# Kernel tuning notes

Measured on AMD Instinct MI355X. Metric: run time of the kernel, lower is better.

The kernel has to match this reference:

```python
import jax, jax.numpy as jnp
import numpy as np

B, L, CH = 8, 32768, 128   # segments, points per segment, channels
H, D = 4, 32               # num_head, ch_head (CH == H*D)
EPS = 1e-5                 # torch GroupNorm default eps


def group_norm1(x, w, b):
    # GroupNorm(num_groups=1, num_channels=CH) applied on [1, CH, L] per segment:
    # normalize over all channels AND points of each segment, then per-channel affine.
    mu = jnp.mean(x, axis=(1, 2), keepdims=True)            # [B,1,1]
    var = jnp.var(x, axis=(1, 2), keepdims=True)            # [B,1,1]
    return (x - mu) * jax.lax.rsqrt(var + EPS) * w + b      # [B,L,CH]


def setup_inputs() -> dict:
    key = jax.random.key(0)
    k0, k1, k2 = jax.random.split(key, 3)
    x = jax.random.normal(k0, (B, L, CH), dtype=jnp.float32)
    W_qkv = jax.random.normal(k1, (CH, 3 * H * D), dtype=jnp.float32) * 0.02
    W_out = jax.random.normal(k2, (H * D, CH), dtype=jnp.float32) * 0.02
    gn1_w = jnp.ones((CH,), jnp.float32)
    gn1_b = jnp.zeros((CH,), jnp.float32)
    gn2_w = jnp.ones((CH,), jnp.float32)
    gn2_b = jnp.zeros((CH,), jnp.float32)
    return {"x": x, "gn1_w": gn1_w, "gn1_b": gn1_b, "W_qkv": W_qkv,
            "W_out": W_out, "gn2_w": gn2_w, "gn2_b": gn2_b}


def reference(x, gn1_w, gn1_b, W_qkv, W_out, gn2_w, gn2_b):
    norm_x = group_norm1(x, gn1_w, gn1_b)                     # [B,L,CH]
    qkv = norm_x @ W_qkv                                      # [B,L,3*H*D]
    q, k, v = jnp.split(qkv, 3, axis=-1)
    q = q.reshape(B, L, H, D)
    k = k.reshape(B, L, H, D)
    v = v.reshape(B, L, H, D)
    # softmax over points within each segment (k / sqrt(segment_len))
    k_soft = jax.nn.softmax(k * (1.0 / np.float32(np.sqrt(L))), axis=1)
    # per-segment, per-head KV context: [B,H,D,D]
    context = jnp.einsum('blhk,blhv->bhkv', k_soft, v)
    # q scaled by ch_head**-0.5, softmax over feature dim
    q_soft = jax.nn.softmax(q * np.float32(D ** -0.5), axis=-1)
    out = jnp.einsum('blhk,bhkv->blhv', q_soft, context).reshape(B, L, H * D)
    out = out @ W_out                                          # [B,L,CH]
    out = group_norm1(out, gn2_w, gn2_b)
    return out + x  # residual
```

## Files before the change

### kernel.cpp

```cpp
#include <hip/hip_runtime.h>

#define NSEG 8
#define LSEG 32768
#define EPS_GN 1e-5f
#define KSCALE 0.005524271728019903f
#define QSCALE 0.17677669529663687f

typedef __attribute__((ext_vector_type(4))) float f32x4;
typedef __attribute__((ext_vector_type(8))) __bf16 bf16x8;
typedef __attribute__((ext_vector_type(4))) short s16x4;

static __device__ __forceinline__ unsigned short f2bf(float f) {
  unsigned int u = __float_as_uint(f);
  u += 0x7fffu + ((u >> 16) & 1u);
  return (unsigned short)(u >> 16);
}
static __device__ __forceinline__ float bf2f(unsigned short s) {
  return __uint_as_float(((unsigned int)s) << 16);
}
static __device__ __forceinline__ bf16x8 cvt8(float4 a, float4 b) {
  bf16x8 r;
  r[0] = (__bf16)a.x; r[1] = (__bf16)a.y; r[2] = (__bf16)a.z; r[3] = (__bf16)a.w;
  r[4] = (__bf16)b.x; r[5] = (__bf16)b.y; r[6] = (__bf16)b.z; r[7] = (__bf16)b.w;
  return r;
}
static __device__ __forceinline__ s16x4 pack4(float a, float b, float c, float d) {
  union { __bf16 h[4]; s16x4 s; } u;
  u.h[0] = (__bf16)a; u.h[1] = (__bf16)b; u.h[2] = (__bf16)c; u.h[3] = (__bf16)d;
  return u.s;
}
static __device__ __forceinline__ ushort4 packu4(f32x4 v) {
  union { __bf16 h[4]; ushort4 u; } u;
  u.h[0] = (__bf16)v[0]; u.h[1] = (__bf16)v[1]; u.h[2] = (__bf16)v[2]; u.h[3] = (__bf16)v[3];
  return u.u;
}

__global__ void k_wcvt(const float* __restrict__ W, const float* __restrict__ gn1w,
                       unsigned short* __restrict__ WT) {
  int idx = blockIdx.x * 256 + threadIdx.x;
  int n = idx >> 7, ch = idx & 127;
  WT[idx] = f2bf(gn1w[ch] * W[ch * 384 + n]);
}

__global__ __launch_bounds__(256) void k_stats1(const float* __restrict__ x, float* __restrict__ part) {
  int t = threadIdx.x;
  int b = blockIdx.x >> 6, p = blockIdx.x & 63;
  const float4* xp = (const float4*)x + (size_t)b * 1048576 + (size_t)p * 16384;
  float s = 0.f, q = 0.f;
  for (int i = 0; i < 64; ++i) {
    float4 v = xp[t + i * 256];
    s += v.x + v.y + v.z + v.w;
    q += v.x*v.x + v.y*v.y + v.z*v.z + v.w*v.w;
  }
  #pragma unroll
  for (int o = 1; o < 64; o <<= 1) { s += __shfl_xor(s, o); q += __shfl_xor(q, o); }
  __shared__ float red[8];
  int wave = t >> 6, lane = t & 63;
  if (lane == 0) { red[wave*2] = s; red[wave*2+1] = q; }
  __syncthreads();
  if (t == 0) {
    part[blockIdx.x*2]   = red[0] + red[2] + red[4] + red[6];
    part[blockIdx.x*2+1] = red[1] + red[3] + red[5] + red[7];
  }
}

__global__ void k_stats1_final(const float* __restrict__ part, float* __restrict__ stats) {
  int b = blockIdx.x, t = threadIdx.x;
  float s = part[(b*64 + t)*2], q = part[(b*64 + t)*2 + 1];
  #pragma unroll
  for (int o = 1; o < 64; o <<= 1) { s += __shfl_xor(s, o); q += __shfl_xor(q, o); }
  if (t == 0) {
    const float invN = 1.f / 4194304.f;
    float mu = s * invN;
    float var = q * invN - mu * mu;
    stats[b*2] = mu;
    stats[b*2+1] = rsqrtf(var + EPS_GN);
  }
}

__global__ void k_bias(const float* __restrict__ Wqkv, const float* __restrict__ gn1w,
                       const float* __restrict__ gn1b, const float* __restrict__ stats1,
                       float* __restrict__ biasv, float* __restrict__ alpha) {
  int seg = blockIdx.x, n = threadIdx.x;
  float mu = stats1[seg*2], rs = stats1[seg*2+1];
  float s = 0.f;
  for (int ch = 0; ch < 128; ++ch)
    s += (gn1b[ch] - mu * rs * gn1w[ch]) * Wqkv[ch * 384 + n];
  float scale = (n < 128) ? QSCALE : ((n < 256) ? KSCALE : 1.f);
  biasv[seg*384 + n] = s * scale;
  if (n == 0) {
    alpha[seg*4]   = rs * QSCALE;
    alpha[seg*4+1] = rs * KSCALE;
    alpha[seg*4+2] = rs;
  }
}

__global__ __launch_bounds__(512, 2) void k_qkv(
    const float* __restrict__ x, const unsigned short* __restrict__ WT,
    const float* __restrict__ biasv, const float* __restrict__ alpha,
    unsigned short* __restrict__ q_ws, float* __restrict__ sume_p, float* __restrict__ ctx_p)
{
  __shared__ float cbuf[4096];
  __shared__ float sume_lds[256];

  const int t = threadIdx.x;
  const int wave = t >> 6, lane = t & 63;
  const int rg = wave >> 2, h = wave & 3;
  const int lm = lane & 15, lg = lane >> 4;
  const int bid = blockIdx.x;
  const int seg = bid >> 5, sub = bid & 31;

  bf16x8 wq[2][4], wk[2][4], wv[2][4];
  #pragma unroll
  for (int nt = 0; nt < 2; ++nt)
    #pragma unroll
    for (int kk = 0; kk < 4; ++kk) {
      int row = h*32 + nt*16 + lm;
      wq[nt][kk] = *(const bf16x8*)&WT[(row      ) * 128 + kk*32 + lg*8];
      wk[nt][kk] = *(const bf16x8*)&WT[(row + 128) * 128 + kk*32 + lg*8];
      wv[nt][kk] = *(const bf16x8*)&WT[(row + 256) * 128 + kk*32 + lg*8];
    }
  const float alk = alpha[seg*4 + 1];
  const float alv = alpha[seg*4 + 2];
  float ckv[2], cvv[2];
  #pragma unroll
  for (int nt = 0; nt < 2; ++nt) {
    ckv[nt] = biasv[seg*384 + 128 + h*32 + nt*16 + lm];
    cvv[nt] = biasv[seg*384 + 256 + h*32 + nt*16 + lm];
  }

  f32x4 ctx00 = {0,0,0,0}, ctx01 = {0,0,0,0}, ctx10 = {0,0,0,0}, ctx11 = {0,0,0,0};
  float se0 = 0.f, se1 = 0.f;

  const float* xw = x + ((size_t)seg * LSEG + sub*1024 + rg*64 + lm) * 128 + lg*8;
  ushort4* q4 = (ushort4*)q_ws;

#define ISSUE(S, IT) { \
    const float* p_ = xw + (size_t)((((IT) >> 2) * 128) + (((IT) & 3) * 16)) * 128; \
    _Pragma("unroll") \
    for (int kk = 0; kk < 4; ++kk) { \
      S[kk][0] = *(const float4*)(p_ + kk*32); \
      S[kk][1] = *(const float4*)(p_ + kk*32 + 4); \
    } }

#define COMPUTE(S, IT) { \
    bf16x8 axf[4]; \
    _Pragma("unroll") for (int kk = 0; kk < 4; ++kk) axf[kk] = cvt8(S[kk][0], S[kk][1]); \
    f32x4 qa0 = {0,0,0,0}, qa1 = {0,0,0,0}; \
    _Pragma("unroll") for (int kk = 0; kk < 4; ++kk) { \
      qa0 = __builtin_amdgcn_mfma_f32_16x16x32_bf16(wq[0][kk], axf[kk], qa0, 0, 0, 0); \
      qa1 = __builtin_amdgcn_mfma_f32_16x16x32_bf16(wq[1][kk], axf[kk], qa1, 0, 0, 0); \
    } \
    { size_t T_ = ((size_t)bid*8 + ((IT) >> 2)) * 64 + (rg*4 + ((IT) & 3)) * 8 + h*2; \
      q4[(T_    ) * 64 + lane] = packu4(qa0); \
      q4[(T_ + 1) * 64 + lane] = packu4(qa1); } \
    f32x4 ka0 = {0,0,0,0}, ka1 = {0,0,0,0}; \
    _Pragma("unroll") for (int kk = 0; kk < 4; ++kk) { \
      ka0 = __builtin_amdgcn_mfma_f32_16x16x32_bf16(axf[kk], wk[0][kk], ka0, 0, 0, 0); \
      ka1 = __builtin_amdgcn_mfma_f32_16x16x32_bf16(axf[kk], wk[1][kk], ka1, 0, 0, 0); \
    } \
    f32x4 va0 = {0,0,0,0}, va1 = {0,0,0,0}; \
    _Pragma("unroll") for (int kk = 0; kk < 4; ++kk) { \
      va0 = __builtin_amdgcn_mfma_f32_16x16x32_bf16(axf[kk], wv[0][kk], va0, 0, 0, 0); \
      va1 = __builtin_amdgcn_mfma_f32_16x16x32_bf16(axf[kk], wv[1][kk], va1, 0, 0, 0); \
    } \
    float e_[8]; \
    _Pragma("unroll") for (int r = 0; r < 4; ++r) e_[r]     = __expf(fmaf(ka0[r], alk, ckv[0])); \
    _Pragma("unroll") for (int r = 0; r < 4; ++r) e_[4 + r] = __expf(fmaf(ka1[r], alk, ckv[1])); \
    se0 += (e_[0] + e_[1]) + (e_[2] + e_[3]); \
    se1 += (e_[4] + e_[5]) + (e_[6] + e_[7]); \
    s16x4 E0 = pack4(e_[0], e_[1], e_[2], e_[3]); \
    s16x4 E1 = pack4(e_[4], e_[5], e_[6], e_[7]); \
    s16x4 V0 = pack4(fmaf(va0[0], alv, cvv[0]), fmaf(va0[1], alv, cvv[0]), \
                     fmaf(va0[2], alv, cvv[0]), fmaf(va0[3], alv, cvv[0])); \
    s16x4 V1 = pack4(fmaf(va1[0], alv, cvv[1]), fmaf(va1[1], alv, cvv[1]), \
                     fmaf(va1[2], alv, cvv[1]), fmaf(va1[3], alv, cvv[1])); \
    ctx00 = __builtin_amdgcn_mfma_f32_16x16x16bf16_1k(E0, V0, ctx00, 0, 0, 0); \
    ctx01 = __builtin_amdgcn_mfma_f32_16x16x16bf16_1k(E0, V1, ctx01, 0, 0, 0); \
    ctx10 = __builtin_amdgcn_mfma_f32_16x16x16bf16_1k(E1, V0, ctx10, 0, 0, 0); \
    ctx11 = __builtin_amdgcn_mfma_f32_16x16x16bf16_1k(E1, V1, ctx11, 0, 0, 0); \
  }

  float4 pa[4][2], pb[4][2];
  ISSUE(pa, 0);
  #pragma unroll 1
  for (int it = 0; it < 32; it += 2) {
    ISSUE(pb, it + 1);
    COMPUTE(pa, it);
    if (it + 2 < 32) ISSUE(pa, it + 2);
    COMPUTE(pb, it + 1);
  }
#undef ISSUE
#undef COMPUTE

  se0 += __shfl_xor(se0, 16); se0 += __shfl_xor(se0, 32);
  se1 += __shfl_xor(se1, 16); se1 += __shfl_xor(se1, 32);
  if (lane < 16) {
    sume_lds[rg*128 + h*32 + lm]      = se0;
    sume_lds[rg*128 + h*32 + 16 + lm] = se1;
  }
  if (rg == 0) {
    #pragma unroll
    for (int r = 0; r < 4; ++r) {
      cbuf[h*1024 + (lg*4 + r)*32      + lm]      = ctx00[r];
      cbuf[h*1024 + (lg*4 + r)*32      + 16 + lm] = ctx01[r];
      cbuf[h*1024 + (16 + lg*4 + r)*32 + lm]      = ctx10[r];
      cbuf[h*1024 + (16 + lg*4 + r)*32 + 16 + lm] = ctx11[r];
    }
  }
  __syncthreads();
  if (rg == 1) {
    #pragma unroll
    for (int r = 0; r < 4; ++r) {
      cbuf[h*1024 + (lg*4 + r)*32      + lm]      += ctx00[r];
      cbuf[h*1024 + (lg*4 + r)*32      + 16 + lm] += ctx01[r];
      cbuf[h*1024 + (16 + lg*4 + r)*32 + lm]      += ctx10[r];
      cbuf[h*1024 + (16 + lg*4 + r)*32 + 16 + lm] += ctx11[r];
    }
  }
  __syncthreads();
  if (t < 128) sume_p[(size_t)bid*128 + t] = sume_lds[t] + sume_lds[128 + t];
  #pragma unroll
  for (int i = 0; i < 8; ++i) {
    int f = t + i * 512;
    ctx_p[(size_t)bid*4096 + f] = cbuf[f];
  }
}

__global__ __launch_bounds__(512) void k_ctx_final(
    const float* __restrict__ sume_p, const float* __restrict__ ctx_p,
    const float* __restrict__ Wout, unsigned short* __restrict__ WcT)
{
  __shared__ float sse[128];
  __shared__ float sctx[4096];
  __shared__ float sWo[16384];
  const int t = threadIdx.x, b = blockIdx.x;
  if (t < 128) {
    float s = 0.f;
    for (int blk = 0; blk < 32; ++blk) s += sume_p[(size_t)(b * 32 + blk) * 128 + t];
    sse[t] = s;
  }
  float cv[8];
  #pragma unroll
  for (int j = 0; j < 8; ++j) {
    int idx = t + j * 512;
    float s = 0.f;
    for (int blk = 0; blk < 32; ++blk) s += ctx_p[(size_t)(b * 32 + blk) * 4096 + idx];
    cv[j] = s;
  }
  #pragma unroll
  for (int j = 0; j < 32; ++j) sWo[t + j * 512] = Wout[t + j * 512];
  __syncthreads();
  #pragma unroll
  for (int j = 0; j < 8; ++j) {
    int idx = t + j * 512;
    sctx[idx] = cv[j] / sse[idx >> 5];
  }
  __syncthreads();
  const int p = t >> 2, c0 = (t & 3) * 32;
  const int h = p >> 5;
  float acc[32];
  #pragma unroll
  for (int j = 0; j < 32; ++j) acc[j] = 0.f;
  for (int v = 0; v < 32; ++v) {
    float a = sctx[p * 32 + v];
    const float* wr = &sWo[(h * 32 + v) * 128 + c0];
    #pragma unroll
    for (int j = 0; j < 32; ++j) acc[j] += a * wr[j];
  }
  #pragma unroll
  for (int j = 0; j < 32; ++j)
    WcT[((size_t)b * 128 + (c0 + j)) * 128 + p] = f2bf(acc[j]);
}

__global__ __launch_bounds__(512) void k_out(
    unsigned short* __restrict__ q_ws, const unsigned short* __restrict__ WcT,
    const float* __restrict__ biasv, const float* __restrict__ alpha,
    float* __restrict__ stats2_p)
{
  __shared__ __attribute__((aligned(16))) unsigned short sWc[128 * 136];
  __shared__ __attribute__((aligned(16))) unsigned char sO[8][16 * 272];
  __shared__ float red[16];

  const int t = threadIdx.x, wave = t >> 6, lane = t & 63;
  const int lm = lane & 15, lg = lane >> 4;
  const int bid = blockIdx.x;
  const int seg = bid >> 8;

  const ushort4* q4c = (const ushort4*)q_ws;
  ushort4 qt[8];
  #pragma unroll
  for (int kt = 0; kt < 8; ++kt)
    qt[kt] = q4c[((size_t)bid * 64 + wave * 8 + kt) * 64 + lane];

  const ushort4* wc4 = (const ushort4*)WcT + (size_t)seg * 4096;
  #pragma unroll
  for (int i = 0; i < 8; ++i) {
    int f = t + i * 512;
    *(ushort4*)&sWc[(f >> 5) * 136 + (f & 31) * 4] = wc4[f];
  }
  const float alq = alpha[seg * 4];
  float4 cq[8];
  #pragma unroll
  for (int kt = 0; kt < 8; ++kt)
    cq[kt] = *(const float4*)&biasv[seg * 384 + kt * 16 + lg * 4];

  __syncthreads();

  s16x4 p[8];
  #pragma unroll
  for (int h = 0; h < 4; ++h) {
    float a[8];
    #pragma unroll
    for (int nt = 0; nt < 2; ++nt) {
      const unsigned short* qe = (const unsigned short*)&qt[2*h + nt];
      const float* cqe = (const float*)&cq[2*h + nt];
      #pragma unroll
      for (int r = 0; r < 4; ++r)
        a[nt*4 + r] = fmaf(bf2f(qe[r]), alq, cqe[r]);
    }
    float m = a[0];
    #pragma unroll
    for (int i = 1; i < 8; ++i) m = fmaxf(m, a[i]);
    m = fmaxf(m, __shfl_xor(m, 16));
    m = fmaxf(m, __shfl_xor(m, 32));
    float s = 0.f;
    #pragma unroll
    for (int i = 0; i < 8; ++i) { a[i] = __expf(a[i] - m); s += a[i]; }
    s += __shfl_xor(s, 16);
    s += __shfl_xor(s, 32);
    float inv = 1.f / s;
    p[2*h]   = pack4(a[0]*inv, a[1]*inv, a[2]*inv, a[3]*inv);
    p[2*h+1] = pack4(a[4]*inv, a[5]*inv, a[6]*inv, a[7]*inv);
  }

  float ssum = 0.f, ssq = 0.f;
  unsigned char* so = &sO[wave][0];
  #pragma unroll
  for (int ot = 0; ot < 8; ++ot) {
    f32x4 acc = {0,0,0,0};
    #pragma unroll
    for (int kt = 0; kt < 8; ++kt) {
      s16x4 wf = *(const s16x4*)&sWc[(ot*16 + lm) * 136 + kt*16 + lg*4];
      acc = __builtin_amdgcn_mfma_f32_16x16x16bf16_1k(wf, p[kt], acc, 0, 0, 0);
    }
    #pragma unroll
    for (int r = 0; r < 4; ++r) { ssum += acc[r]; ssq += acc[r] * acc[r]; }
    *(ushort4*)(so + lm * 272 + ot * 32 + lg * 8) = packu4(acc);
  }
  #pragma unroll
  for (int i = 0; i < 4; ++i) {
    int row = i * 4 + (lane >> 4);
    float4 v = *(const float4*)(so + row * 272 + (lane & 15) * 16);
    *(float4*)((char*)q_ws + ((size_t)bid * 128 + wave * 16 + row) * 256 + (lane & 15) * 16) = v;
  }

  #pragma unroll
  for (int o = 1; o < 64; o <<= 1) { ssum += __shfl_xor(ssum, o); ssq += __shfl_xor(ssq, o); }
  if (lane == 0) { red[wave*2] = ssum; red[wave*2+1] = ssq; }
  __syncthreads();
  if (t == 0) {
    float s = 0.f, q = 0.f;
    #pragma unroll
    for (int w = 0; w < 8; ++w) { s += red[w*2]; q += red[w*2+1]; }
    stats2_p[bid*2] = s; stats2_p[bid*2+1] = q;
  }
}

__global__ void k_stats2_final(const float* __restrict__ part, float* __restrict__ stats) {
  int b = blockIdx.x, t = threadIdx.x;
  float s = part[(b*256 + t)*2], q = part[(b*256 + t)*2 + 1];
  #pragma unroll
  for (int o = 1; o < 64; o <<= 1) { s += __shfl_xor(s, o); q += __shfl_xor(q, o); }
  __shared__ float red[8];
  int wave = t >> 6, lane = t & 63;
  if (lane == 0) { red[wave*2] = s; red[wave*2+1] = q; }
  __syncthreads();
  if (t == 0) {
    float ss = red[0] + red[2] + red[4] + red[6];
    float qq = red[1] + red[3] + red[5] + red[7];
    const float invN = 1.f / 4194304.f;
    float mu = ss * invN;
    float var = qq * invN - mu * mu;
    stats[b*2] = mu;
    stats[b*2+1] = rsqrtf(var + EPS_GN);
  }
}

__global__ __launch_bounds__(256) void k_final(
    const float* __restrict__ x, const unsigned short* __restrict__ out_ws,
    const float* __restrict__ stats2, const float* __restrict__ gn2w, const float* __restrict__ gn2b,
    float* __restrict__ y)
{
  const int t = threadIdx.x;
  const int b = blockIdx.x >> 8, blk = blockIdx.x & 255;
  const float mu = stats2[b*2], rs = stats2[b*2+1];
  const int c4 = t & 31;
  const float4 w4 = *(const float4*)&gn2w[c4*4];
  const float4 g4 = *(const float4*)&gn2b[c4*4];
  const size_t base = (size_t)b * 1048576 + (size_t)blk * 4096;
  const float4* xp = (const float4*)x + base;
  const ushort4* op = (const ushort4*)out_ws + base;
  float4* yp = (float4*)y + base;
  #pragma unroll
  for (int i = 0; i < 16; ++i) {
    int f = t + i * 256;
    float4 xv = xp[f];
    ushort4 ov = op[f];
    float4 r;
    r.x = (bf2f(ov.x) - mu) * rs * w4.x + g4.x + xv.x;
    r.y = (bf2f(ov.y) - mu) * rs * w4.y + g4.y + xv.y;
    r.z = (bf2f(ov.z) - mu) * rs * w4.z + g4.z + xv.z;
    r.w = (bf2f(ov.w) - mu) * rs * w4.w + g4.w + xv.w;
    yp[f] = r;
  }
}

extern "C" void kernel_launch(void* const* d_in, const int* in_sizes, int n_in,
                              void* d_out, int out_size, void* d_ws, size_t ws_size,
                              hipStream_t stream) {
  const float* x    = (const float*)d_in[0];
  const float* gn1w = (const float*)d_in[1];
  const float* gn1b = (const float*)d_in[2];
  const float* Wqkv = (const float*)d_in[3];
  const float* Wout = (const float*)d_in[4];
  const float* gn2w = (const float*)d_in[5];
  const float* gn2b = (const float*)d_in[6];
  float* y = (float*)d_out;
  char* ws = (char*)d_ws;

  float*          stats1p = (float*)(ws + 0);
  float*          stats1  = (float*)(ws + 4096);
  unsigned short* WT      = (unsigned short*)(ws + 8192);
  float*          biasv   = (float*)(ws + 106496);
  float*          alphav  = (float*)(ws + 118784);
  float*          sume_p  = (float*)(ws + 122880);
  float*          ctx_p   = (float*)(ws + 253952);
  unsigned short* WcT     = (unsigned short*)(ws + 4448256);
  float*          stats2p = (float*)(ws + 4710400);
  float*          stats2  = (float*)(ws + 4726784);
  unsigned short* q_ws    = (unsigned short*)(ws + 4849664);

  hipLaunchKernelGGL(k_wcvt,         dim3(192),  dim3(256), 0, stream, Wqkv, gn1w, WT);
  hipLaunchKernelGGL(k_stats1,       dim3(512),  dim3(256), 0, stream, x, stats1p);
  hipLaunchKernelGGL(k_stats1_final, dim3(8),    dim3(64),  0, stream, stats1p, stats1);
  hipLaunchKernelGGL(k_bias,         dim3(8),    dim3(384), 0, stream, Wqkv, gn1w, gn1b, stats1, biasv, alphav);
  hipLaunchKernelGGL(k_qkv,          dim3(256),  dim3(512), 0, stream, x, WT, biasv, alphav, q_ws, sume_p, ctx_p);
  hipLaunchKernelGGL(k_ctx_final,    dim3(8),    dim3(512), 0, stream, sume_p, ctx_p, Wout, WcT);
  hipLaunchKernelGGL(k_out,          dim3(2048), dim3(512), 0, stream, q_ws, WcT, biasv, alphav, stats2p);
  hipLaunchKernelGGL(k_stats2_final, dim3(8),    dim3(256), 0, stream, stats2p, stats2);
  hipLaunchKernelGGL(k_final,        dim3(2048), dim3(256), 0, stream, x, q_ws, stats2, gn2w, gn2b, y);
}
```

Before: 214.0 us.

## Cache bf16 copy of x, fuse stat reductions, move q softmax into QKV kernel

The first-pass statistics kernel now also writes a bf16 copy of x and absorbs the weight conversion. The QKV and final kernels read that half-width copy instead of re-reading fp32 x. The separate stats-finalize kernels are folded into their consumers, and the q feature softmax moves from k_out into k_qkv. k_qkv is also retiled to 256-thread blocks with a four-deep load pipeline and no LDS reduction. The aim is less HBM traffic and fewer launches, at the cost of adding the residual from a bf16-rounded x, which lowers output accuracy.

```diff
diff --git a/kernel.cpp b/kernel.cpp
--- a/kernel.cpp
+++ b/kernel.cpp
@@ -10,6 +10,9 @@
 typedef __attribute__((ext_vector_type(8))) __bf16 bf16x8;
 typedef __attribute__((ext_vector_type(4))) short s16x4;
 
+#define MFMA32(A, B, C) __builtin_amdgcn_mfma_f32_16x16x32_bf16(A, B, C, 0, 0, 0)
+#define MFMA16(A, B, C) __builtin_amdgcn_mfma_f32_16x16x16bf16_1k(A, B, C, 0, 0, 0)
+
 static __device__ __forceinline__ unsigned short f2bf(float f) {
   unsigned int u = __float_as_uint(f);
   u += 0x7fffu + ((u >> 16) & 1u);
@@ -18,39 +21,35 @@
 static __device__ __forceinline__ float bf2f(unsigned short s) {
   return __uint_as_float(((unsigned int)s) << 16);
 }
-static __device__ __forceinline__ bf16x8 cvt8(float4 a, float4 b) {
-  bf16x8 r;
-  r[0] = (__bf16)a.x; r[1] = (__bf16)a.y; r[2] = (__bf16)a.z; r[3] = (__bf16)a.w;
-  r[4] = (__bf16)b.x; r[5] = (__bf16)b.y; r[6] = (__bf16)b.z; r[7] = (__bf16)b.w;
-  return r;
-}
 static __device__ __forceinline__ s16x4 pack4(float a, float b, float c, float d) {
   union { __bf16 h[4]; s16x4 s; } u;
   u.h[0] = (__bf16)a; u.h[1] = (__bf16)b; u.h[2] = (__bf16)c; u.h[3] = (__bf16)d;
   return u.s;
 }
-static __device__ __forceinline__ ushort4 packu4(f32x4 v) {
-  union { __bf16 h[4]; ushort4 u; } u;
-  u.h[0] = (__bf16)v[0]; u.h[1] = (__bf16)v[1]; u.h[2] = (__bf16)v[2]; u.h[3] = (__bf16)v[3];
-  return u.u;
-}
-
-__global__ void k_wcvt(const float* __restrict__ W, const float* __restrict__ gn1w,
-                       unsigned short* __restrict__ WT) {
-  int idx = blockIdx.x * 256 + threadIdx.x;
-  int n = idx >> 7, ch = idx & 127;
-  WT[idx] = f2bf(gn1w[ch] * W[ch * 384 + n]);
-}
-
-__global__ __launch_bounds__(256) void k_stats1(const float* __restrict__ x, float* __restrict__ part) {
-  int t = threadIdx.x;
-  int b = blockIdx.x >> 6, p = blockIdx.x & 63;
+static __device__ __forceinline__ s16x4 as_s16x4(ushort4 v) {
+  union { ushort4 u; s16x4 s; } c; c.u = v; return c.s;
+}
+
+__global__ __launch_bounds__(256) void k_pre(
+    const float* __restrict__ x, float* __restrict__ part, unsigned short* __restrict__ xb,
+    const float* __restrict__ W, const float* __restrict__ gn1w, unsigned short* __restrict__ WT)
+{
+  const int t = threadIdx.x;
+  if (blockIdx.x >= 512) {
+    int idx = (blockIdx.x - 512) * 256 + t;
+    int n = idx >> 7, ch = idx & 127;
+    WT[idx] = f2bf(gn1w[ch] * W[ch * 384 + n]);
+    return;
+  }
+  const int b = blockIdx.x >> 6, p = blockIdx.x & 63;
   const float4* xp = (const float4*)x + (size_t)b * 1048576 + (size_t)p * 16384;
+  ushort4* xo = (ushort4*)xb + (size_t)b * 1048576 + (size_t)p * 16384;
   float s = 0.f, q = 0.f;
   for (int i = 0; i < 64; ++i) {
     float4 v = xp[t + i * 256];
     s += v.x + v.y + v.z + v.w;
     q += v.x*v.x + v.y*v.y + v.z*v.z + v.w*v.w;
+    xo[t + i * 256] = make_ushort4(f2bf(v.x), f2bf(v.y), f2bf(v.z), f2bf(v.w));
   }
   #pragma unroll
   for (int o = 1; o < 64; o <<= 1) { s += __shfl_xor(s, o); q += __shfl_xor(q, o); }
@@ -64,51 +63,46 @@
   }
 }
 
-__global__ void k_stats1_final(const float* __restrict__ part, float* __restrict__ stats) {
-  int b = blockIdx.x, t = threadIdx.x;
-  float s = part[(b*64 + t)*2], q = part[(b*64 + t)*2 + 1];
-  #pragma unroll
-  for (int o = 1; o < 64; o <<= 1) { s += __shfl_xor(s, o); q += __shfl_xor(q, o); }
-  if (t == 0) {
-    const float invN = 1.f / 4194304.f;
-    float mu = s * invN;
-    float var = q * invN - mu * mu;
-    stats[b*2] = mu;
-    stats[b*2+1] = rsqrtf(var + EPS_GN);
-  }
-}
-
 __global__ void k_bias(const float* __restrict__ Wqkv, const float* __restrict__ gn1w,
-                       const float* __restrict__ gn1b, const float* __restrict__ stats1,
+                       const float* __restrict__ gn1b, const float* __restrict__ part,
                        float* __restrict__ biasv, float* __restrict__ alpha) {
-  int seg = blockIdx.x, n = threadIdx.x;
-  float mu = stats1[seg*2], rs = stats1[seg*2+1];
+  const int seg = blockIdx.x, t = threadIdx.x;
+  __shared__ float sm[2];
+  if (t < 64) {
+    float s = part[(seg*64 + t)*2], q = part[(seg*64 + t)*2 + 1];
+    #pragma unroll
+    for (int o = 1; o < 64; o <<= 1) { s += __shfl_xor(s, o); q += __shfl_xor(q, o); }
+    if (t == 0) {
+      const float invN = 1.f / 4194304.f;
+      float mu = s * invN;
+      float var = q * invN - mu * mu;
+      sm[0] = mu; sm[1] = rsqrtf(var + EPS_GN);
+    }
+  }
+  __syncthreads();
+  const float mu = sm[0], rs = sm[1];
   float s = 0.f;
   for (int ch = 0; ch < 128; ++ch)
-    s += (gn1b[ch] - mu * rs * gn1w[ch]) * Wqkv[ch * 384 + n];
-  float scale = (n < 128) ? QSCALE : ((n < 256) ? KSCALE : 1.f);
-  biasv[seg*384 + n] = s * scale;
-  if (n == 0) {
+    s += (gn1b[ch] - mu * rs * gn1w[ch]) * Wqkv[ch * 384 + t];
+  float scale = (t < 128) ? QSCALE : ((t < 256) ? KSCALE : 1.f);
+  biasv[seg*384 + t] = s * scale;
+  if (t == 0) {
     alpha[seg*4]   = rs * QSCALE;
     alpha[seg*4+1] = rs * KSCALE;
     alpha[seg*4+2] = rs;
   }
 }
 
-__global__ __launch_bounds__(512, 2) void k_qkv(
-    const float* __restrict__ x, const unsigned short* __restrict__ WT,
+__global__ __launch_bounds__(256, 2) void k_qkv(
+    const unsigned short* __restrict__ xb, const unsigned short* __restrict__ WT,
     const float* __restrict__ biasv, const float* __restrict__ alpha,
     unsigned short* __restrict__ q_ws, float* __restrict__ sume_p, float* __restrict__ ctx_p)
 {
-  __shared__ float cbuf[4096];
-  __shared__ float sume_lds[256];
-
   const int t = threadIdx.x;
-  const int wave = t >> 6, lane = t & 63;
-  const int rg = wave >> 2, h = wave & 3;
+  const int h = t >> 6, lane = t & 63;
   const int lm = lane & 15, lg = lane >> 4;
   const int bid = blockIdx.x;
-  const int seg = bid >> 5, sub = bid & 31;
+  const int seg = bid >> 6, sub = bid & 63;
 
   bf16x8 wq[2][4], wk[2][4], wv[2][4];
   #pragma unroll
@@ -120,75 +114,90 @@
       wk[nt][kk] = *(const bf16x8*)&WT[(row + 128) * 128 + kk*32 + lg*8];
       wv[nt][kk] = *(const bf16x8*)&WT[(row + 256) * 128 + kk*32 + lg*8];
     }
-  const float alk = alpha[seg*4 + 1];
-  const float alv = alpha[seg*4 + 2];
-  float ckv[2], cvv[2];
-  #pragma unroll
-  for (int nt = 0; nt < 2; ++nt) {
-    ckv[nt] = biasv[seg*384 + 128 + h*32 + nt*16 + lm];
-    cvv[nt] = biasv[seg*384 + 256 + h*32 + nt*16 + lm];
-  }
+  const float alq = alpha[seg*4], alk = alpha[seg*4 + 1], alv = alpha[seg*4 + 2];
+  const float4 cq0 = *(const float4*)&biasv[seg*384 + h*32 +      lg*4];
+  const float4 cq1 = *(const float4*)&biasv[seg*384 + h*32 + 16 + lg*4];
+  const float ck0 = biasv[seg*384 + 128 + h*32 + lm];
+  const float ck1 = biasv[seg*384 + 128 + h*32 + 16 + lm];
+  const float cv0 = biasv[seg*384 + 256 + h*32 + lm];
+  const float cv1 = biasv[seg*384 + 256 + h*32 + 16 + lm];
 
   f32x4 ctx00 = {0,0,0,0}, ctx01 = {0,0,0,0}, ctx10 = {0,0,0,0}, ctx11 = {0,0,0,0};
   float se0 = 0.f, se1 = 0.f;
 
-  const float* xw = x + ((size_t)seg * LSEG + sub*1024 + rg*64 + lm) * 128 + lg*8;
+  const unsigned short* xw = xb + (size_t)(seg * LSEG + sub*512 + lm) * 128 + lg*8;
   ushort4* q4 = (ushort4*)q_ws;
 
 #define ISSUE(S, IT) { \
-    const float* p_ = xw + (size_t)((((IT) >> 2) * 128) + (((IT) & 3) * 16)) * 128; \
-    _Pragma("unroll") \
-    for (int kk = 0; kk < 4; ++kk) { \
-      S[kk][0] = *(const float4*)(p_ + kk*32); \
-      S[kk][1] = *(const float4*)(p_ + kk*32 + 4); \
-    } }
+    const unsigned short* p_ = xw + (size_t)((((IT) >> 3) * 128) + (((IT) & 7) * 16)) * 128; \
+    S[0] = *(const bf16x8*)(p_);      \
+    S[1] = *(const bf16x8*)(p_ + 32); \
+    S[2] = *(const bf16x8*)(p_ + 64); \
+    S[3] = *(const bf16x8*)(p_ + 96); }
 
 #define COMPUTE(S, IT) { \
-    bf16x8 axf[4]; \
-    _Pragma("unroll") for (int kk = 0; kk < 4; ++kk) axf[kk] = cvt8(S[kk][0], S[kk][1]); \
     f32x4 qa0 = {0,0,0,0}, qa1 = {0,0,0,0}; \
     _Pragma("unroll") for (int kk = 0; kk < 4; ++kk) { \
-      qa0 = __builtin_amdgcn_mfma_f32_16x16x32_bf16(wq[0][kk], axf[kk], qa0, 0, 0, 0); \
-      qa1 = __builtin_amdgcn_mfma_f32_16x16x32_bf16(wq[1][kk], axf[kk], qa1, 0, 0, 0); \
+      qa0 = MFMA32(wq[0][kk], S[kk], qa0); \
+      qa1 = MFMA32(wq[1][kk], S[kk], qa1); \
     } \
-    { size_t T_ = ((size_t)bid*8 + ((IT) >> 2)) * 64 + (rg*4 + ((IT) & 3)) * 8 + h*2; \
-      q4[(T_    ) * 64 + lane] = packu4(qa0); \
-      q4[(T_ + 1) * 64 + lane] = packu4(qa1); } \
-    f32x4 ka0 = {0,0,0,0}, ka1 = {0,0,0,0}; \
+    float a_[8]; \
+    _Pragma("unroll") for (int r = 0; r < 4; ++r) { \
+      a_[r]     = fmaf(qa0[r], alq, ((const float*)&cq0)[r]); \
+      a_[4 + r] = fmaf(qa1[r], alq, ((const float*)&cq1)[r]); \
+    } \
+    float m_ = a_[0]; \
+    _Pragma("unroll") for (int i = 1; i < 8; ++i) m_ = fmaxf(m_, a_[i]); \
+    m_ = fmaxf(m_, __shfl_xor(m_, 16)); \
+    m_ = fmaxf(m_, __shfl_xor(m_, 32)); \
+    float s_ = 0.f; \
+    _Pragma("unroll") for (int i = 0; i < 8; ++i) { a_[i] = __expf(a_[i] - m_); s_ += a_[i]; } \
+    s_ += __shfl_xor(s_, 16); \
+    s_ += __shfl_xor(s_, 32); \
+    float inv_ = 1.f / s_; \
+    { size_t T_ = ((size_t)(bid*4 + ((IT) >> 3))) * 64 + ((IT) & 7) * 8 + h*2; \
+      q4[T_*64 + lane]     = make_ushort4(f2bf(a_[0]*inv_), f2bf(a_[1]*inv_), f2bf(a_[2]*inv_), f2bf(a_[3]*inv_)); \
+      q4[(T_+1)*64 + lane] = make_ushort4(f2bf(a_[4]*inv_), f2bf(a_[5]*inv_), f2bf(a_[6]*inv_), f2bf(a_[7]*inv_)); } \
+    f32x4 ka0 = {0,0,0,0}, ka1 = {0,0,0,0}, va0 = {0,0,0,0}, va1 = {0,0,0,0}; \
     _Pragma("unroll") for (int kk = 0; kk < 4; ++kk) { \
-      ka0 = __builtin_amdgcn_mfma_f32_16x16x32_bf16(axf[kk], wk[0][kk], ka0, 0, 0, 0); \
-      ka1 = __builtin_amdgcn_mfma_f32_16x16x32_bf16(axf[kk], wk[1][kk], ka1, 0, 0, 0); \
+      ka0 = MFMA32(S[kk], wk[0][kk], ka0); \
+      ka1 = MFMA32(S[kk], wk[1][kk], ka1); \
     } \
-    f32x4 va0 = {0,0,0,0}, va1 = {0,0,0,0}; \
     _Pragma("unroll") for (int kk = 0; kk < 4; ++kk) { \
-      va0 = __builtin_amdgcn_mfma_f32_16x16x32_bf16(axf[kk], wv[0][kk], va0, 0, 0, 0); \
-      va1 = __builtin_amdgcn_mfma_f32_16x16x32_bf16(axf[kk], wv[1][kk], va1, 0, 0, 0); \
+      va0 = MFMA32(S[kk], wv[0][kk], va0); \
+      va1 = MFMA32(S[kk], wv[1][kk], va1); \
     } \
     float e_[8]; \
-    _Pragma("unroll") for (int r = 0; r < 4; ++r) e_[r]     = __expf(fmaf(ka0[r], alk, ckv[0])); \
-    _Pragma("unroll") for (int r = 0; r < 4; ++r) e_[4 + r] = __expf(fmaf(ka1[r], alk, ckv[1])); \
+    _Pragma("unroll") for (int r = 0; r < 4; ++r) { \
+      e_[r]     = __expf(fmaf(ka0[r], alk, ck0)); \
+      e_[4 + r] = __expf(fmaf(ka1[r], alk, ck1)); \
+    } \
     se0 += (e_[0] + e_[1]) + (e_[2] + e_[3]); \
     se1 += (e_[4] + e_[5]) + (e_[6] + e_[7]); \
     s16x4 E0 = pack4(e_[0], e_[1], e_[2], e_[3]); \
     s16x4 E1 = pack4(e_[4], e_[5], e_[6], e_[7]); \
-    s16x4 V0 = pack4(fmaf(va0[0], alv, cvv[0]), fmaf(va0[1], alv, cvv[0]), \
-                     fmaf(va0[2], alv, cvv[0]), fmaf(va0[3], alv, cvv[0])); \
-    s16x4 V1 = pack4(fmaf(va1[0], alv, cvv[1]), fmaf(va1[1], alv, cvv[1]), \
-                     fmaf(va1[2], alv, cvv[1]), fmaf(va1[3], alv, cvv[1])); \
-    ctx00 = __builtin_amdgcn_mfma_f32_16x16x16bf16_1k(E0, V0, ctx00, 0, 0, 0); \
-    ctx01 = __builtin_amdgcn_mfma_f32_16x16x16bf16_1k(E0, V1, ctx01, 0, 0, 0); \
-    ctx10 = __builtin_amdgcn_mfma_f32_16x16x16bf16_1k(E1, V0, ctx10, 0, 0, 0); \
-    ctx11 = __builtin_amdgcn_mfma_f32_16x16x16bf16_1k(E1, V1, ctx11, 0, 0, 0); \
-  }
-
-  float4 pa[4][2], pb[4][2];
-  ISSUE(pa, 0);
+    s16x4 V0 = pack4(fmaf(va0[0], alv, cv0), fmaf(va0[1], alv, cv0), \
+                     fmaf(va0[2], alv, cv0), fmaf(va0[3], alv, cv0)); \
+    s16x4 V1 = pack4(fmaf(va1[0], alv, cv1), fmaf(va1[1], alv, cv1), \
+                     fmaf(va1[2], alv, cv1), fmaf(va1[3], alv, cv1)); \
+    ctx00 = MFMA16(E0, V0, ctx00); \
+    ctx01 = MFMA16(E0, V1, ctx01); \
+    ctx10 = MFMA16(E1, V0, ctx10); \
+    ctx11 = MFMA16(E1, V1, ctx11); }
+
+  bf16x8 sA[4], sB[4], sC[4], sD[4];
+  ISSUE(sA, 0);
+  ISSUE(sB, 1);
   #pragma unroll 1
-  for (int it = 0; it < 32; it += 2) {
-    ISSUE(pb, it + 1);
-    COMPUTE(pa, it);
-    if (it + 2 < 32) ISSUE(pa, it + 2);
-    COMPUTE(pb, it + 1);
+  for (int it = 0; it < 32; it += 4) {
+    ISSUE(sC, it + 2);
+    COMPUTE(sA, it);
+    ISSUE(sD, it + 3);
+    COMPUTE(sB, it + 1);
+    if (it + 4 < 32) ISSUE(sA, it + 4);
+    COMPUTE(sC, it + 2);
+    if (it + 5 < 32) ISSUE(sB, it + 5);
+    COMPUTE(sD, it + 3);
   }
 #undef ISSUE
 #undef COMPUTE
@@ -196,34 +205,16 @@
   se0 += __shfl_xor(se0, 16); se0 += __shfl_xor(se0, 32);
   se1 += __shfl_xor(se1, 16); se1 += __shfl_xor(se1, 32);
   if (lane < 16) {
-    sume_lds[rg*128 + h*32 + lm]      = se0;
-    sume_lds[rg*128 + h*32 + 16 + lm] = se1;
-  }
-  if (rg == 0) {
-    #pragma unroll
-    for (int r = 0; r < 4; ++r) {
-      cbuf[h*1024 + (lg*4 + r)*32      + lm]      = ctx00[r];
-      cbuf[h*1024 + (lg*4 + r)*32      + 16 + lm] = ctx01[r];
-      cbuf[h*1024 + (16 + lg*4 + r)*32 + lm]      = ctx10[r];
-      cbuf[h*1024 + (16 + lg*4 + r)*32 + 16 + lm] = ctx11[r];
-    }
-  }
-  __syncthreads();
-  if (rg == 1) {
-    #pragma unroll
-    for (int r = 0; r < 4; ++r) {
-      cbuf[h*1024 + (lg*4 + r)*32      + lm]      += ctx00[r];
-      cbuf[h*1024 + (lg*4 + r)*32      + 16 + lm] += ctx01[r];
-      cbuf[h*1024 + (16 + lg*4 + r)*32 + lm]      += ctx10[r];
-      cbuf[h*1024 + (16 + lg*4 + r)*32 + 16 + lm] += ctx11[r];
-    }
-  }
-  __syncthreads();
-  if (t < 128) sume_p[(size_t)bid*128 + t] = sume_lds[t] + sume_lds[128 + t];
-  #pragma unroll
-  for (int i = 0; i < 8; ++i) {
-    int f = t + i * 512;
-    ctx_p[(size_t)bid*4096 + f] = cbuf[f];
+    sume_p[(size_t)bid*128 + h*32 + lm]      = se0;
+    sume_p[(size_t)bid*128 + h*32 + 16 + lm] = se1;
+  }
+  float* cp = ctx_p + (size_t)bid*4096 + h*1024;
+  #pragma unroll
+  for (int r = 0; r < 4; ++r) {
+    cp[(lg*4 + r)*32      + lm]      = ctx00[r];
+    cp[(lg*4 + r)*32      + 16 + lm] = ctx01[r];
+    cp[(16 + lg*4 + r)*32 + lm]      = ctx10[r];
+    cp[(16 + lg*4 + r)*32 + 16 + lm] = ctx11[r];
   }
 }
 
@@ -237,7 +228,7 @@
   const int t = threadIdx.x, b = blockIdx.x;
   if (t < 128) {
     float s = 0.f;
-    for (int blk = 0; blk < 32; ++blk) s += sume_p[(size_t)(b * 32 + blk) * 128 + t];
+    for (int blk = 0; blk < 64; ++blk) s += sume_p[(size_t)(b * 64 + blk) * 128 + t];
     sse[t] = s;
   }
   float cv[8];
@@ -245,7 +236,7 @@
   for (int j = 0; j < 8; ++j) {
     int idx = t + j * 512;
     float s = 0.f;
-    for (int blk = 0; blk < 32; ++blk) s += ctx_p[(size_t)(b * 32 + blk) * 4096 + idx];
+    for (int blk = 0; blk < 64; ++blk) s += ctx_p[(size_t)(b * 64 + blk) * 4096 + idx];
     cv[j] = s;
   }
   #pragma unroll
@@ -275,7 +266,6 @@
 
 __global__ __launch_bounds__(512) void k_out(
     unsigned short* __restrict__ q_ws, const unsigned short* __restrict__ WcT,
-    const float* __restrict__ biasv, const float* __restrict__ alpha,
     float* __restrict__ stats2_p)
 {
   __shared__ __attribute__((aligned(16))) unsigned short sWc[128 * 136];
@@ -288,10 +278,10 @@
   const int seg = bid >> 8;
 
   const ushort4* q4c = (const ushort4*)q_ws;
-  ushort4 qt[8];
+  s16x4 p[8];
   #pragma unroll
   for (int kt = 0; kt < 8; ++kt)
-    qt[kt] = q4c[((size_t)bid * 64 + wave * 8 + kt) * 64 + lane];
+    p[kt] = as_s16x4(q4c[((size_t)bid * 64 + wave * 8 + kt) * 64 + lane]);
 
   const ushort4* wc4 = (const ushort4*)WcT + (size_t)seg * 4096;
   #pragma unroll
@@ -299,40 +289,7 @@
     int f = t + i * 512;
     *(ushort4*)&sWc[(f >> 5) * 136 + (f & 31) * 4] = wc4[f];
   }
-  const float alq = alpha[seg * 4];
-  float4 cq[8];
-  #pragma unroll
-  for (int kt = 0; kt < 8; ++kt)
-    cq[kt] = *(const float4*)&biasv[seg * 384 + kt * 16 + lg * 4];
-
-  __syncthreads();
-
-  s16x4 p[8];
-  #pragma unroll
-  for (int h = 0; h < 4; ++h) {
-    float a[8];
-    #pragma unroll
-    for (int nt = 0; nt < 2; ++nt) {
-      const unsigned short* qe = (const unsigned short*)&qt[2*h + nt];
-      const float* cqe = (const float*)&cq[2*h + nt];
-      #pragma unroll
-      for (int r = 0; r < 4; ++r)
-        a[nt*4 + r] = fmaf(bf2f(qe[r]), alq, cqe[r]);
-    }
-    float m = a[0];
-    #pragma unroll
-    for (int i = 1; i < 8; ++i) m = fmaxf(m, a[i]);
-    m = fmaxf(m, __shfl_xor(m, 16));
-    m = fmaxf(m, __shfl_xor(m, 32));
-    float s = 0.f;
-    #pragma unroll
-    for (int i = 0; i < 8; ++i) { a[i] = __expf(a[i] - m); s += a[i]; }
-    s += __shfl_xor(s, 16);
-    s += __shfl_xor(s, 32);
-    float inv = 1.f / s;
-    p[2*h]   = pack4(a[0]*inv, a[1]*inv, a[2]*inv, a[3]*inv);
-    p[2*h+1] = pack4(a[4]*inv, a[5]*inv, a[6]*inv, a[7]*inv);
-  }
+  __syncthreads();
 
   float ssum = 0.f, ssq = 0.f;
   unsigned char* so = &sO[wave][0];
@@ -342,11 +299,12 @@
     #pragma unroll
     for (int kt = 0; kt < 8; ++kt) {
       s16x4 wf = *(const s16x4*)&sWc[(ot*16 + lm) * 136 + kt*16 + lg*4];
-      acc = __builtin_amdgcn_mfma_f32_16x16x16bf16_1k(wf, p[kt], acc, 0, 0, 0);
+      acc = MFMA16(wf, p[kt], acc);
     }
     #pragma unroll
     for (int r = 0; r < 4; ++r) { ssum += acc[r]; ssq += acc[r] * acc[r]; }
-    *(ushort4*)(so + lm * 272 + ot * 32 + lg * 8) = packu4(acc);
+    *(ushort4*)(so + lm * 272 + ot * 32 + lg * 8) =
+        make_ushort4(f2bf(acc[0]), f2bf(acc[1]), f2bf(acc[2]), f2bf(acc[3]));
   }
   #pragma unroll
   for (int i = 0; i < 4; ++i) {
@@ -367,51 +325,50 @@
   }
 }
 
-__global__ void k_stats2_final(const float* __restrict__ part, float* __restrict__ stats) {
-  int b = blockIdx.x, t = threadIdx.x;
-  float s = part[(b*256 + t)*2], q = part[(b*256 + t)*2 + 1];
-  #pragma unroll
-  for (int o = 1; o < 64; o <<= 1) { s += __shfl_xor(s, o); q += __shfl_xor(q, o); }
-  __shared__ float red[8];
-  int wave = t >> 6, lane = t & 63;
-  if (lane == 0) { red[wave*2] = s; red[wave*2+1] = q; }
-  __syncthreads();
-  if (t == 0) {
-    float ss = red[0] + red[2] + red[4] + red[6];
-    float qq = red[1] + red[3] + red[5] + red[7];
-    const float invN = 1.f / 4194304.f;
-    float mu = ss * invN;
-    float var = qq * invN - mu * mu;
-    stats[b*2] = mu;
-    stats[b*2+1] = rsqrtf(var + EPS_GN);
-  }
-}
-
 __global__ __launch_bounds__(256) void k_final(
-    const float* __restrict__ x, const unsigned short* __restrict__ out_ws,
-    const float* __restrict__ stats2, const float* __restrict__ gn2w, const float* __restrict__ gn2b,
+    const unsigned short* __restrict__ xb, const unsigned short* __restrict__ out_ws,
+    const float* __restrict__ stats2_p, const float* __restrict__ gn2w, const float* __restrict__ gn2b,
     float* __restrict__ y)
 {
+  __shared__ float red[8];
+  __shared__ float sm[2];
   const int t = threadIdx.x;
   const int b = blockIdx.x >> 8, blk = blockIdx.x & 255;
-  const float mu = stats2[b*2], rs = stats2[b*2+1];
+  {
+    float s = stats2_p[(b*256 + t)*2], q = stats2_p[(b*256 + t)*2 + 1];
+    #pragma unroll
+    for (int o = 1; o < 64; o <<= 1) { s += __shfl_xor(s, o); q += __shfl_xor(q, o); }
+    int wave = t >> 6, lane = t & 63;
+    if (lane == 0) { red[wave*2] = s; red[wave*2+1] = q; }
+    __syncthreads();
+    if (t == 0) {
+      float ss = red[0] + red[2] + red[4] + red[6];
+      float qq = red[1] + red[3] + red[5] + red[7];
+      const float invN = 1.f / 4194304.f;
+      float mu = ss * invN;
+      float var = qq * invN - mu * mu;
+      sm[0] = mu; sm[1] = rsqrtf(var + EPS_GN);
+    }
+    __syncthreads();
+  }
+  const float mu = sm[0], rs = sm[1];
   const int c4 = t & 31;
   const float4 w4 = *(const float4*)&gn2w[c4*4];
   const float4 g4 = *(const float4*)&gn2b[c4*4];
   const size_t base = (size_t)b * 1048576 + (size_t)blk * 4096;
-  const float4* xp = (const float4*)x + base;
+  const ushort4* xp = (const ushort4*)xb + base;
   const ushort4* op = (const ushort4*)out_ws + base;
   float4* yp = (float4*)y + base;
   #pragma unroll
   for (int i = 0; i < 16; ++i) {
     int f = t + i * 256;
-    float4 xv = xp[f];
+    ushort4 xv = xp[f];
     ushort4 ov = op[f];
     float4 r;
-    r.x = (bf2f(ov.x) - mu) * rs * w4.x + g4.x + xv.x;
-    r.y = (bf2f(ov.y) - mu) * rs * w4.y + g4.y + xv.y;
-    r.z = (bf2f(ov.z) - mu) * rs * w4.z + g4.z + xv.z;
-    r.w = (bf2f(ov.w) - mu) * rs * w4.w + g4.w + xv.w;
+    r.x = (bf2f(ov.x) - mu) * rs * w4.x + g4.x + bf2f(xv.x);
+    r.y = (bf2f(ov.y) - mu) * rs * w4.y + g4.y + bf2f(xv.y);
+    r.z = (bf2f(ov.z) - mu) * rs * w4.z + g4.z + bf2f(xv.z);
+    r.w = (bf2f(ov.w) - mu) * rs * w4.w + g4.w + bf2f(xv.w);
     yp[f] = r;
   }
 }
@@ -429,25 +386,21 @@
   float* y = (float*)d_out;
   char* ws = (char*)d_ws;
 
-  float*          stats1p = (float*)(ws + 0);
-  float*          stats1  = (float*)(ws + 4096);
+  float*          part    = (float*)(ws + 0);
   unsigned short* WT      = (unsigned short*)(ws + 8192);
   float*          biasv   = (float*)(ws + 106496);
   float*          alphav  = (float*)(ws + 118784);
   float*          sume_p  = (float*)(ws + 122880);
-  float*          ctx_p   = (float*)(ws + 253952);
-  unsigned short* WcT     = (unsigned short*)(ws + 4448256);
-  float*          stats2p = (float*)(ws + 4710400);
-  float*          stats2  = (float*)(ws + 4726784);
-  unsigned short* q_ws    = (unsigned short*)(ws + 4849664);
-
-  hipLaunchKernelGGL(k_wcvt,         dim3(192),  dim3(256), 0, stream, Wqkv, gn1w, WT);
-  hipLaunchKernelGGL(k_stats1,       dim3(512),  dim3(256), 0, stream, x, stats1p);
-  hipLaunchKernelGGL(k_stats1_final, dim3(8),    dim3(64),  0, stream, stats1p, stats1);
-  hipLaunchKernelGGL(k_bias,         dim3(8),    dim3(384), 0, stream, Wqkv, gn1w, gn1b, stats1, biasv, alphav);
-  hipLaunchKernelGGL(k_qkv,          dim3(256),  dim3(512), 0, stream, x, WT, biasv, alphav, q_ws, sume_p, ctx_p);
-  hipLaunchKernelGGL(k_ctx_final,    dim3(8),    dim3(512), 0, stream, sume_p, ctx_p, Wout, WcT);
-  hipLaunchKernelGGL(k_out,          dim3(2048), dim3(512), 0, stream, q_ws, WcT, biasv, alphav, stats2p);
-  hipLaunchKernelGGL(k_stats2_final, dim3(8),    dim3(256), 0, stream, stats2p, stats2);
-  hipLaunchKernelGGL(k_final,        dim3(2048), dim3(256), 0, stream, x, q_ws, stats2, gn2w, gn2b, y);
-}
+  float*          ctx_p   = (float*)(ws + 385024);
+  unsigned short* WcT     = (unsigned short*)(ws + 8773632);
+  float*          stats2p = (float*)(ws + 9035776);
+  unsigned short* xb      = (unsigned short*)(ws + 9052160);
+  unsigned short* q_ws    = (unsigned short*)(ws + 76161024);
+
+  hipLaunchKernelGGL(k_pre,       dim3(704),  dim3(256), 0, stream, x, part, xb, Wqkv, gn1w, WT);
+  hipLaunchKernelGGL(k_bias,      dim3(8),    dim3(384), 0, stream, Wqkv, gn1w, gn1b, part, biasv, alphav);
+  hipLaunchKernelGGL(k_qkv,       dim3(512),  dim3(256), 0, stream, xb, WT, biasv, alphav, q_ws, sume_p, ctx_p);
+  hipLaunchKernelGGL(k_ctx_final, dim3(8),    dim3(512), 0, stream, sume_p, ctx_p, Wout, WcT);
+  hipLaunchKernelGGL(k_out,       dim3(2048), dim3(512), 0, stream, q_ws, WcT, stats2p);
+  hipLaunchKernelGGL(k_final,     dim3(2048), dim3(256), 0, stream, xb, q_ws, stats2p, gn2w, gn2b, y);
+}
```

Result: no change. 211.1 us (-1.4%).
